# Performance work log

Measured on AMD Instinct MI355X. Metric: run time of the kernel, lower is better.

The kernel has to match this reference:

```python
import jax, jax.numpy as jnp
import numpy as np

K = 3
TOP_K = 10
MASK_RATIO = 0.5
EPS_COS = 1e-8
EPS_DEG = 1e-6


def setup_inputs() -> dict:
    key = jax.random.key(0)
    ks = jax.random.split(key, 10)
    N, C, H, O, E = 4096, 128, 128, 64, 65536
    x = jax.random.normal(ks[0], (N, C), dtype=jnp.float32)
    edge_index = jax.random.randint(ks[1], (2, E), 0, N, dtype=jnp.int64)
    alpha = jnp.full((K,), 1.0 / K, dtype=jnp.float32)
    fusion_W = 0.02 * jax.random.normal(ks[2], (2 * H, H), dtype=jnp.float32)
    fusion_b = jnp.zeros((H,), dtype=jnp.float32)
    lin0_W = 0.02 * jax.random.normal(ks[3], (C, H), dtype=jnp.float32)
    lin0_b = jnp.zeros((H,), dtype=jnp.float32)
    lin1_W = 0.02 * jax.random.normal(ks[4], (H, O), dtype=jnp.float32)
    lin1_b = jnp.zeros((O,), dtype=jnp.float32)
    return {
        "x": x, "edge_index": edge_index, "alpha": alpha,
        "fusion_W": fusion_W, "fusion_b": fusion_b,
        "lin0_W": lin0_W, "lin0_b": lin0_b,
        "lin1_W": lin1_W, "lin1_b": lin1_b,
    }


def reference(x, edge_index, alpha, fusion_W, fusion_b, lin0_W, lin0_b, lin1_W, lin1_b):
    N = x.shape[0]
    # dense adjacency and its powers: A^0 = I (so A^0 @ x = x), A^1, A^2
    A = jnp.zeros((N, N), x.dtype).at[edge_index[0], edge_index[1]].set(1.0)
    A2 = A @ A
    hop_feats = jnp.stack([x, A @ x, A2 @ x], axis=0)  # [K, N, C]

    # per-node cosine-similarity top-k (self always included, cos=1)
    xn = x / (jnp.linalg.norm(x, axis=-1, keepdims=True) + EPS_COS)
    sim = xn @ xn.T  # [N, N]
    _, topk_idx = jax.lax.top_k(sim, TOP_K)  # [N, TOP_K]

    # random keep-mask per node, forced True at top-k neighbors
    mask = jax.random.uniform(jax.random.key(42), (N, N)) < MASK_RATIO
    rows = jnp.arange(N)[:, None]
    mask = mask.at[rows, topk_idx].set(True)
    Mf = mask.astype(x.dtype)  # [N, N]

    # alpha-weighted multi-hop aggregate, masked mean over selected nodes
    agg = jnp.einsum('k,knc->nc', alpha, hop_feats)  # [N, C]
    fused = (Mf @ agg) / (Mf.sum(axis=1, keepdims=True) + EPS_DEG)  # [N, C]

    h = jnp.concatenate([x, fused], axis=-1) @ fusion_W + fusion_b
    h = jax.nn.relu(h @ lin0_W + lin0_b)  # dropout inactive in eval
    out = h @ lin1_W + lin1_b
    return jax.nn.log_softmax(out, axis=1)
```

## Files before the change

### kernel.cpp

```cpp
#include <hip/hip_runtime.h>
#include <hip/hip_bf16.h>
#include <stdint.h>


#define N_NODES 4096
#define C_DIM   128
#define WPR     128
#define HALF_P  8388608u
#define TOPK    10
#define LSTR    13
#define JSPLIT  4
#define KSPLIT  2

typedef __attribute__((ext_vector_type(8))) short bf16x8;
typedef __attribute__((ext_vector_type(4))) float f32x4;

__device__ __forceinline__ uint16_t f2bf(float f) {
    uint32_t u = __float_as_uint(f);
    return (uint16_t)((u + 0x7FFFu + ((u >> 16) & 1u)) >> 16);
}

__device__ __forceinline__ uint32_t rotl32(uint32_t v, int r) {
    return (v << r) | (v >> (32 - r));
}

__device__ __forceinline__ void threefry2x32(uint32_t k0, uint32_t k1,
                                             uint32_t x0, uint32_t x1,
                                             uint32_t& o0, uint32_t& o1) {
    uint32_t ks2 = k0 ^ k1 ^ 0x1BD11BDAu;
    x0 += k0; x1 += k1;
#define TF_ROUND(r) { x0 += x1; x1 = rotl32(x1, (r)); x1 ^= x0; }
    TF_ROUND(13) TF_ROUND(15) TF_ROUND(26) TF_ROUND(6)
    x0 += k1;  x1 += ks2 + 1u;
    TF_ROUND(17) TF_ROUND(29) TF_ROUND(16) TF_ROUND(24)
    x0 += ks2; x1 += k0 + 2u;
    TF_ROUND(13) TF_ROUND(15) TF_ROUND(26) TF_ROUND(6)
    x0 += k0;  x1 += k1 + 3u;
    TF_ROUND(17) TF_ROUND(29) TF_ROUND(16) TF_ROUND(24)
    x0 += k1;  x1 += ks2 + 4u;
    TF_ROUND(13) TF_ROUND(15) TF_ROUND(26) TF_ROUND(6)
    x0 += ks2; x1 += k0 + 5u;
#undef TF_ROUND
    o0 = x0; o1 = x1;
}

__global__ void scatter_kernel(const int* __restrict__ ei, int E,
                               uint32_t* __restrict__ Abits) {
    __shared__ int cnt_oddnz;
    int t = threadIdx.x;
    if (t == 0) cnt_oddnz = 0;
    __syncthreads();
    if (((const uint32_t*)ei)[2 * t + 1] != 0u) atomicAdd(&cnt_oddnz, 1);
    __syncthreads();
    bool is64 = (cnt_oddnz <= 8);
    int e = blockIdx.x * blockDim.x + t;
    if (e >= E) return;
    int src, dst;
    if (is64) { src = ei[2 * e]; dst = ei[2 * (E + e)]; }
    else      { src = ei[e];     dst = ei[E + e]; }
    src &= (N_NODES - 1);
    dst &= (N_NODES - 1);
    atomicOr(&Abits[src * WPR + (dst >> 5)], 1u << (dst & 31));
}

__global__ void spmm_norm_kernel(const uint32_t* __restrict__ Abits,
                                 const float* __restrict__ xf,
                                 float* __restrict__ hop1,
                                 uint16_t* __restrict__ xnb) {
    int i = blockIdx.x;
    int c = threadIdx.x;
    __shared__ uint32_t wbits[WPR];
    __shared__ float ws[2];
    wbits[c] = Abits[i * WPR + c];
    __syncthreads();
    float acc = 0.f;
    for (int w = 0; w < WPR; ++w) {
        uint32_t bits = wbits[w];
        while (bits) {
            int b = __ffs(bits) - 1;
            bits &= bits - 1;
            acc += xf[(w * 32 + b) * C_DIM + c];
        }
    }
    hop1[i * C_DIM + c] = acc;
    float v = xf[i * C_DIM + c];
    float sq = v * v;
    #pragma unroll
    for (int off = 32; off >= 1; off >>= 1) sq += __shfl_xor(sq, off);
    if ((c & 63) == 0) ws[c >> 6] = sq;
    __syncthreads();
    float tot = ws[0] + ws[1];
    xnb[i * C_DIM + c] = f2bf(v / (sqrtf(tot) + 1e-8f));
}

__launch_bounds__(512, 4)
__global__ void combo_topk_kernel(const uint32_t* __restrict__ Abits,
                                  const float* __restrict__ hop1,
                                  const float* __restrict__ xf,
                                  const float* __restrict__ alpha,
                                  uint16_t* __restrict__ aggTb,
                                  const uint16_t* __restrict__ xnb,
                                  uint32_t* __restrict__ Mbits,
                                  int* __restrict__ degInt,
                                  float* __restrict__ topv,
                                  int* __restrict__ topi) {
    __shared__ uint8_t smem[32 * 16 * LSTR * 6];
    int t = threadIdx.x;

    if (blockIdx.x < 1024) {
        float*    sval = (float*)smem;
        uint16_t* sidx = (uint16_t*)(smem + 32 * 16 * LSTR * 4);
        int it   = blockIdx.x & 255;
        int part = blockIdx.x >> 8;
        int i0 = it * 16;
        int w = t >> 6;
        int lane = t & 63;
        int col = lane & 15;
        int quad = lane >> 4;

        bf16x8 bfi[4];
        #pragma unroll
        for (int s = 0; s < 4; ++s)
            bfi[s] = *(const bf16x8*)&xnb[(size_t)(i0 + col) * C_DIM + s * 32 + quad * 8];

        float tv[TOPK]; int ti[TOPK];
        #pragma unroll
        for (int k = 0; k < TOPK; ++k) { tv[k] = -1e30f; ti[k] = 0xFFFF; }

        int jt0 = part * 64 + w * 8;
        for (int p = 0; p < 8; ++p) {
            int j0 = (jt0 + p) * 16;
            f32x4 acc = {0.f, 0.f, 0.f, 0.f};
            #pragma unroll
            for (int s = 0; s < 4; ++s) {
                bf16x8 aj = *(const bf16x8*)&xnb[(size_t)(j0 + col) * C_DIM + s * 32 + quad * 8];
                acc = __builtin_amdgcn_mfma_f32_16x16x32_bf16(aj, bfi[s], acc, 0, 0, 0);
            }
            float m4 = fmaxf(fmaxf(acc[0], acc[1]), fmaxf(acc[2], acc[3]));
            if (m4 > tv[TOPK-1]) {
                #pragma unroll
                for (int r = 0; r < 4; ++r) {
                    float d = acc[r];
                    if (d > tv[TOPK-1]) {
                        int j = j0 + quad * 4 + r;
                        tv[TOPK-1] = d; ti[TOPK-1] = j;
                        #pragma unroll
                        for (int q = TOPK - 2; q >= 0; --q) {
                            if (tv[q+1] > tv[q]) {
                                float fv = tv[q]; tv[q] = tv[q+1]; tv[q+1] = fv;
                                int iv = ti[q];  ti[q] = ti[q+1];  ti[q+1] = iv;
                            }
                        }
                    }
                }
            }
        }

        int base = ((w * 4 + quad) * 16 + col) * LSTR;
        #pragma unroll
        for (int k = 0; k < TOPK; ++k) {
            sval[base + k] = tv[k];
            sidx[base + k] = (uint16_t)ti[k];
        }

        int row = t & 15, L = t >> 4;
        for (int s = 16; s >= 1; s >>= 1) {
            __syncthreads();
            if (L < s) {
                int la = (L * 16 + row) * LSTR;
                int lb = ((L + s) * 16 + row) * LSTR;
                float ov[TOPK]; uint16_t oi[TOPK];
                int ia = 0, ib = 0;
                #pragma unroll
                for (int k = 0; k < TOPK; ++k) {
                    float va = sval[la + ia], vb = sval[lb + ib];
                    uint16_t xa = sidx[la + ia], xb = sidx[lb + ib];
                    bool takeA = (va > vb) || (va == vb && xa < xb);
                    if (takeA) { ov[k] = va; oi[k] = xa; ++ia; }
                    else       { ov[k] = vb; oi[k] = xb; ++ib; }
                }
                #pragma unroll
                for (int k = 0; k < TOPK; ++k) { sval[la + k] = ov[k]; sidx[la + k] = oi[k]; }
            }
        }
        __syncthreads();
        if (t < 16) {
            size_t gi = (size_t)(part * N_NODES + i0 + t) * TOPK;
            #pragma unroll
            for (int k = 0; k < TOPK; ++k) {
                topv[gi + k] = sval[t * LSTR + k];
                topi[gi + k] = (int)sidx[t * LSTR + k];
            }
        }
    } else {
        uint32_t* wb = (uint32_t*)smem;
        int bid = blockIdx.x - 1024;
        int sg = t >> 7;
        int c  = t & 127;
        int i  = bid * 4 + sg;
        wb[sg * 128 + c] = Abits[i * WPR + c];
        __syncthreads();
        float acc = 0.f;
        for (int w = 0; w < WPR; ++w) {
            uint32_t bits = wb[sg * 128 + w];
            while (bits) {
                int b = __ffs(bits) - 1;
                bits &= bits - 1;
                acc += hop1[(w * 32 + b) * C_DIM + c];
            }
        }
        float xv  = xf[i * C_DIM + c];
        float h1v = hop1[i * C_DIM + c];
        float a = alpha[0] * xv + alpha[1] * h1v + alpha[2] * acc;
        aggTb[(size_t)c * N_NODES + i] = f2bf(a);

        uint32_t u = (uint32_t)(i * 128 + c);
        uint32_t tid = u >> 1;
        uint32_t halfb = u & 1u;
        uint32_t base = tid * 32u + halfb * 16u;
        uint32_t w0 = 0u, w1 = 0u;
        for (int k = 0; k < 16; ++k) {
            uint32_t o0, o1;
            threefry2x32(0u, 42u, base + k, HALF_P + base + k, o0, o1);
            w0 |= (uint32_t)((o0 >> 31) ^ 1u) << k;
            w1 |= (uint32_t)((o1 >> 31) ^ 1u) << k;
        }
        uint32_t w0o = (uint32_t)__shfl_xor((int)w0, 1);
        uint32_t w1o = (uint32_t)__shfl_xor((int)w1, 1);
        int p0 = 0, p1 = 0;
        if (halfb == 0u) {
            uint32_t W0 = w0 | (w0o << 16);
            uint32_t W1 = w1 | (w1o << 16);
            Mbits[tid] = W0;
            Mbits[(HALF_P >> 5) + tid] = W1;
            p0 = __popc(W0); p1 = __popc(W1);
        }
        #pragma unroll
        for (int off = 32; off >= 1; off >>= 1) {
            p0 += __shfl_xor(p0, off);
            p1 += __shfl_xor(p1, off);
        }
        if ((t & 63) == 0) {
            int row0 = i >> 1;
            atomicAdd(&degInt[row0], p0);
            atomicAdd(&degInt[2048 + row0], p1);
        }
    }
}

__launch_bounds__(512, 4)
__global__ void fused_kernel(const uint32_t* __restrict__ Mbits,
                             const uint16_t* __restrict__ aggTb,
                             const float* __restrict__ topv,
                             const int* __restrict__ topi,
                             int* __restrict__ degInt,
                             float* __restrict__ fpart) {
    int i0 = blockIdx.x * 16;
    int part = blockIdx.y;
    int t = threadIdx.x;
    int w = t >> 6;
    int lane = t & 63;
    int col = lane & 15;
    int quad = lane >> 4;

    __shared__ uint32_t smask[16][65];
    __shared__ float    lv[16][JSPLIT][TOPK];
    __shared__ uint16_t li[16][JSPLIT][TOPK];
    for (int r = t; r < 16 * 64; r += 512)
        smask[r >> 6][r & 63] =
            Mbits[(size_t)(i0 + (r >> 6)) * WPR + part * 64 + (r & 63)];
    if (t < 16 * JSPLIT) {
        int row = t & 15, q = t >> 4;
        size_t gi = (size_t)(q * N_NODES + i0 + row) * TOPK;
        #pragma unroll
        for (int k = 0; k < TOPK; ++k) {
            lv[row][q][k] = topv[gi + k];
            li[row][q][k] = (uint16_t)topi[gi + k];
        }
    }
    __syncthreads();

    if (t < 16) {
        int ix[JSPLIT] = {0, 0, 0, 0};
        int newc = 0;
        int kw0 = part * 2048;
        #pragma unroll
        for (int k = 0; k < TOPK; ++k) {
            float bestv = -1e38f; int bestj = 0x7fffffff; int bestq = 0;
            #pragma unroll
            for (int q = 0; q < JSPLIT; ++q) {
                bool ok = ix[q] < TOPK;
                float fv = ok ? lv[t][q][ix[q]] : -1e38f;
                int   jj = ok ? (int)li[t][q][ix[q]] : 0x7fffffff;
                if (fv > bestv || (fv == bestv && jj < bestj)) {
                    bestv = fv; bestj = jj; bestq = q;
                }
            }
            ++ix[bestq];
            int rel = bestj - kw0;
            if (rel >= 0 && rel < 2048) {
                uint32_t* wp = &smask[t][rel >> 5];
                uint32_t old = *wp, bit = 1u << (bestj & 31);
                newc += (int)((old & bit) == 0u);
                *wp = old | bit;
            }
        }
        if (newc) atomicAdd(&degInt[i0 + t], newc);
    }
    __syncthreads();

    const uint16_t* brow = aggTb + (size_t)(w * 16 + col) * N_NODES;
    int kbase = part * 2048;
    f32x4 acc[4];
    #pragma unroll
    for (int u = 0; u < 4; ++u) acc[u] = (f32x4){0.f, 0.f, 0.f, 0.f};

    for (int k0 = 0; k0 < 2048; k0 += 128) {
        #pragma unroll
        for (int u = 0; u < 4; ++u) {
            uint32_t mw = smask[col][(k0 >> 5) + u];
            uint32_t byte = (mw >> (quad * 8)) & 0xFFu;
            union { uint32_t uu[4]; bf16x8 v; } a;
            #pragma unroll
            for (int pp = 0; pp < 4; ++pp) {
                uint32_t lo = (byte >> (2 * pp)) & 1u;
                uint32_t hi = (byte >> (2 * pp + 1)) & 1u;
                a.uu[pp] = (lo ? 0x3F80u : 0u) | (hi ? 0x3F800000u : 0u);
            }
            bf16x8 b = *(const bf16x8*)&brow[kbase + k0 + u * 32 + quad * 8];
            acc[u] = __builtin_amdgcn_mfma_f32_16x16x32_bf16(a.v, b, acc[u], 0, 0, 0);
        }
    }
    #pragma unroll
    for (int r = 0; r < 4; ++r) {
        int il = quad * 4 + r;
        float s = (acc[0][r] + acc[1][r]) + (acc[2][r] + acc[3][r]);
        fpart[(size_t)part * (N_NODES * C_DIM)
              + (size_t)(i0 + il) * C_DIM + w * 16 + col] = s;
    }
}

__global__ void mlp_kernel(const float* __restrict__ xf,
                           const float* __restrict__ fpart,
                           const int* __restrict__ degInt,
                           const float* __restrict__ fW, const float* __restrict__ fB,
                           const float* __restrict__ l0W, const float* __restrict__ l0B,
                           const float* __restrict__ l1W, const float* __restrict__ l1B,
                           float* __restrict__ out) {
    int i0 = blockIdx.x * 4;
    int t = threadIdx.x;
    __shared__ float lx[4][256];
    __shared__ float hb[4][128];
    const float* f0 = fpart;
    const float* f1 = fpart + (size_t)N_NODES * C_DIM;
    for (int r = t; r < 4 * 128; r += 128) {
        int row = r >> 7, c = r & 127;
        size_t idx = (size_t)(i0 + row) * C_DIM + c;
        lx[row][c] = xf[idx];
        lx[row][128 + c] = (f0[idx] + f1[idx])
                           / ((float)degInt[i0 + row] + 1e-6f);
    }
    __syncthreads();
    float acc[4];
    #pragma unroll
    for (int r = 0; r < 4; ++r) acc[r] = fB[t];
    for (int k = 0; k < 256; ++k) {
        float wv = fW[k * 128 + t];
        #pragma unroll
        for (int r = 0; r < 4; ++r) acc[r] = fmaf(lx[r][k], wv, acc[r]);
    }
    #pragma unroll
    for (int r = 0; r < 4; ++r) hb[r][t] = acc[r];
    __syncthreads();
    #pragma unroll
    for (int r = 0; r < 4; ++r) acc[r] = l0B[t];
    for (int k = 0; k < 128; ++k) {
        float wv = l0W[k * 128 + t];
        #pragma unroll
        for (int r = 0; r < 4; ++r) acc[r] = fmaf(hb[r][k], wv, acc[r]);
    }
    __syncthreads();
    #pragma unroll
    for (int r = 0; r < 4; ++r) lx[r][t] = fmaxf(acc[r], 0.f);
    __syncthreads();
    int o = t & 63, pr = t >> 6;
    #pragma unroll
    for (int rr = 0; rr < 2; ++rr) {
        int r = pr + 2 * rr;
        float a = l1B[o];
        for (int k = 0; k < 128; ++k)
            a = fmaf(lx[r][k], l1W[k * 64 + o], a);
        float m = a;
        #pragma unroll
        for (int off = 32; off >= 1; off >>= 1) m = fmaxf(m, __shfl_xor(m, off));
        float e = expf(a - m);
        float s = e;
        #pragma unroll
        for (int off = 32; off >= 1; off >>= 1) s += __shfl_xor(s, off);
        out[(size_t)(i0 + r) * 64 + o] = a - m - logf(s);
    }
}

extern "C" void kernel_launch(void* const* d_in, const int* in_sizes, int n_in,
                              void* d_out, int out_size, void* d_ws, size_t ws_size,
                              hipStream_t stream) {
    const float* xf    = (const float*)d_in[0];
    const int*   ei    = (const int*)d_in[1];
    const float* alpha = (const float*)d_in[2];
    const float* fW    = (const float*)d_in[3];
    const float* fB    = (const float*)d_in[4];
    const float* l0W   = (const float*)d_in[5];
    const float* l0B   = (const float*)d_in[6];
    const float* l1W   = (const float*)d_in[7];
    const float* l1B   = (const float*)d_in[8];
    float* out = (float*)d_out;
    const int E  = in_sizes[1] / 2;
    const int NC = N_NODES * C_DIM;

    char* p = (char*)d_ws;
    const size_t SZ = (size_t)NC * 4;
    uint32_t* Abits  = (uint32_t*)p; p += SZ;
    int*      degInt = (int*)p;      p += N_NODES * 4;
    float*    hop1   = (float*)p;    p += SZ;
    uint32_t* Mbits  = (uint32_t*)p; p += SZ;
    float*    fpart  = (float*)p;    p += KSPLIT * SZ;
    uint16_t* xnb    = (uint16_t*)p; p += SZ / 2;
    uint16_t* aggTb  = (uint16_t*)p; p += SZ / 2;
    float*    topv   = (float*)p;    p += (size_t)JSPLIT * N_NODES * TOPK * 4;
    int*      topi   = (int*)p;      p += (size_t)JSPLIT * N_NODES * TOPK * 4;

    hipMemsetAsync(Abits, 0, SZ + N_NODES * 4, stream);
    scatter_kernel<<<(E + 255) / 256, 256, 0, stream>>>(ei, E, Abits);
    spmm_norm_kernel<<<N_NODES, 128, 0, stream>>>(Abits, xf, hop1, xnb);
    combo_topk_kernel<<<2048, 512, 0, stream>>>(Abits, hop1, xf, alpha,
                                                aggTb, xnb, Mbits, degInt,
                                                topv, topi);
    fused_kernel<<<dim3(N_NODES / 16, KSPLIT), 512, 0, stream>>>(Mbits, aggTb,
                                                                 topv, topi,
                                                                 degInt, fpart);
    mlp_kernel<<<N_NODES / 4, 128, 0, stream>>>(xf, fpart, degInt,
                                                fW, fB, l0W, l0B, l1W, l1B, out);
}
```

Baseline: 226.6 us.

## Merge memset, scatter, spmm and combo/topk into one cooperative kernel

Replaces the memset, scatter, first-hop SpMM/normalize and combo/topk launches with a single cooperative mega-kernel of 1024 blocks that uses grid.sync between phases. The aim is to remove launch and inter-kernel gaps. In exchange, the topk and hop2 phases, previously split across 2048 blocks, now run sequentially within each block. The launch bounds rise to 8 waves so all blocks can be co-resident, which risks register pressure in the topk code, and grid-wide barriers add their own cost.

```diff
diff --git a/kernel.cpp b/kernel.cpp
--- a/kernel.cpp
+++ b/kernel.cpp
@@ -1,7 +1,10 @@
 #include <hip/hip_runtime.h>
 #include <hip/hip_bf16.h>
+#include <hip/hip_cooperative_groups.h>
 #include <stdint.h>
 
+
+namespace cg = cooperative_groups;
 
 #define N_NODES 4096
 #define C_DIM   128
@@ -44,74 +47,83 @@
     o0 = x0; o1 = x1;
 }
 
-__global__ void scatter_kernel(const int* __restrict__ ei, int E,
-                               uint32_t* __restrict__ Abits) {
+__launch_bounds__(512, 8)
+__global__ void mega_kernel(const int* __restrict__ ei, int E,
+                            const float* __restrict__ xf,
+                            const float* __restrict__ alpha,
+                            uint32_t* __restrict__ Abits,
+                            int* __restrict__ degInt,
+                            float* __restrict__ hop1,
+                            uint16_t* __restrict__ xnb,
+                            uint16_t* __restrict__ aggTb,
+                            uint32_t* __restrict__ Mbits,
+                            float* __restrict__ topv,
+                            int* __restrict__ topi) {
+    cg::grid_group grid = cg::this_grid();
+    __shared__ uint8_t smem[32 * 16 * LSTR * 6];
+    __shared__ float ws4[4][2];
     __shared__ int cnt_oddnz;
     int t = threadIdx.x;
-    if (t == 0) cnt_oddnz = 0;
-    __syncthreads();
-    if (((const uint32_t*)ei)[2 * t + 1] != 0u) atomicAdd(&cnt_oddnz, 1);
-    __syncthreads();
-    bool is64 = (cnt_oddnz <= 8);
-    int e = blockIdx.x * blockDim.x + t;
-    if (e >= E) return;
-    int src, dst;
-    if (is64) { src = ei[2 * e]; dst = ei[2 * (E + e)]; }
-    else      { src = ei[e];     dst = ei[E + e]; }
-    src &= (N_NODES - 1);
-    dst &= (N_NODES - 1);
-    atomicOr(&Abits[src * WPR + (dst >> 5)], 1u << (dst & 31));
-}
-
-__global__ void spmm_norm_kernel(const uint32_t* __restrict__ Abits,
-                                 const float* __restrict__ xf,
-                                 float* __restrict__ hop1,
-                                 uint16_t* __restrict__ xnb) {
-    int i = blockIdx.x;
-    int c = threadIdx.x;
-    __shared__ uint32_t wbits[WPR];
-    __shared__ float ws[2];
-    wbits[c] = Abits[i * WPR + c];
-    __syncthreads();
-    float acc = 0.f;
-    for (int w = 0; w < WPR; ++w) {
-        uint32_t bits = wbits[w];
-        while (bits) {
-            int b = __ffs(bits) - 1;
-            bits &= bits - 1;
-            acc += xf[(w * 32 + b) * C_DIM + c];
-        }
-    }
-    hop1[i * C_DIM + c] = acc;
-    float v = xf[i * C_DIM + c];
-    float sq = v * v;
-    #pragma unroll
-    for (int off = 32; off >= 1; off >>= 1) sq += __shfl_xor(sq, off);
-    if ((c & 63) == 0) ws[c >> 6] = sq;
-    __syncthreads();
-    float tot = ws[0] + ws[1];
-    xnb[i * C_DIM + c] = f2bf(v / (sqrtf(tot) + 1e-8f));
-}
-
-__launch_bounds__(512, 4)
-__global__ void combo_topk_kernel(const uint32_t* __restrict__ Abits,
-                                  const float* __restrict__ hop1,
-                                  const float* __restrict__ xf,
-                                  const float* __restrict__ alpha,
-                                  uint16_t* __restrict__ aggTb,
-                                  const uint16_t* __restrict__ xnb,
-                                  uint32_t* __restrict__ Mbits,
-                                  int* __restrict__ degInt,
-                                  float* __restrict__ topv,
-                                  int* __restrict__ topi) {
-    __shared__ uint8_t smem[32 * 16 * LSTR * 6];
-    int t = threadIdx.x;
-
-    if (blockIdx.x < 1024) {
+    int b = blockIdx.x;
+
+    {
+        int total = N_NODES * WPR + N_NODES;
+        for (int idx = b * 512 + t; idx < total; idx += 1024 * 512)
+            Abits[idx] = 0u;
+    }
+    grid.sync();
+
+    {
+        if (t == 0) cnt_oddnz = 0;
+        __syncthreads();
+        if (t < 256 && ((const uint32_t*)ei)[2 * t + 1] != 0u)
+            atomicAdd(&cnt_oddnz, 1);
+        __syncthreads();
+        bool is64 = (cnt_oddnz <= 8);
+        int e = b * 64 + t;
+        if (t < 64 && e < E) {
+            int src, dst;
+            if (is64) { src = ei[2 * e]; dst = ei[2 * (E + e)]; }
+            else      { src = ei[e];     dst = ei[E + e]; }
+            src &= (N_NODES - 1);
+            dst &= (N_NODES - 1);
+            atomicOr(&Abits[src * WPR + (dst >> 5)], 1u << (dst & 31));
+        }
+    }
+    grid.sync();
+
+    {
+        uint32_t* wb = (uint32_t*)smem;
+        int sg = t >> 7, c = t & 127;
+        int i = b * 4 + sg;
+        wb[sg * 128 + c] = Abits[i * WPR + c];
+        __syncthreads();
+        float acc = 0.f;
+        for (int w = 0; w < WPR; ++w) {
+            uint32_t bits = wb[sg * 128 + w];
+            while (bits) {
+                int bb = __ffs(bits) - 1;
+                bits &= bits - 1;
+                acc += xf[(w * 32 + bb) * C_DIM + c];
+            }
+        }
+        hop1[i * C_DIM + c] = acc;
+        float v = xf[i * C_DIM + c];
+        float sq = v * v;
+        #pragma unroll
+        for (int off = 32; off >= 1; off >>= 1) sq += __shfl_xor(sq, off);
+        if ((c & 63) == 0) ws4[sg][c >> 6] = sq;
+        __syncthreads();
+        float tot = ws4[sg][0] + ws4[sg][1];
+        xnb[i * C_DIM + c] = f2bf(v / (sqrtf(tot) + 1e-8f));
+    }
+    grid.sync();
+
+    {
         float*    sval = (float*)smem;
         uint16_t* sidx = (uint16_t*)(smem + 32 * 16 * LSTR * 4);
-        int it   = blockIdx.x & 255;
-        int part = blockIdx.x >> 8;
+        int it   = b & 255;
+        int part = b >> 8;
         int i0 = it * 16;
         int w = t >> 6;
         int lane = t & 63;
@@ -192,21 +204,23 @@
                 topi[gi + k] = (int)sidx[t * LSTR + k];
             }
         }
-    } else {
+        __syncthreads();
+    }
+
+    {
         uint32_t* wb = (uint32_t*)smem;
-        int bid = blockIdx.x - 1024;
         int sg = t >> 7;
         int c  = t & 127;
-        int i  = bid * 4 + sg;
+        int i  = b * 4 + sg;
         wb[sg * 128 + c] = Abits[i * WPR + c];
         __syncthreads();
         float acc = 0.f;
         for (int w = 0; w < WPR; ++w) {
             uint32_t bits = wb[sg * 128 + w];
             while (bits) {
-                int b = __ffs(bits) - 1;
+                int bb = __ffs(bits) - 1;
                 bits &= bits - 1;
-                acc += hop1[(w * 32 + b) * C_DIM + c];
+                acc += hop1[(w * 32 + bb) * C_DIM + c];
             }
         }
         float xv  = xf[i * C_DIM + c];
@@ -327,8 +341,8 @@
                 uint32_t hi = (byte >> (2 * pp + 1)) & 1u;
                 a.uu[pp] = (lo ? 0x3F80u : 0u) | (hi ? 0x3F800000u : 0u);
             }
-            bf16x8 b = *(const bf16x8*)&brow[kbase + k0 + u * 32 + quad * 8];
-            acc[u] = __builtin_amdgcn_mfma_f32_16x16x32_bf16(a.v, b, acc[u], 0, 0, 0);
+            bf16x8 bvec = *(const bf16x8*)&brow[kbase + k0 + u * 32 + quad * 8];
+            acc[u] = __builtin_amdgcn_mfma_f32_16x16x32_bf16(a.v, bvec, acc[u], 0, 0, 0);
         }
     }
     #pragma unroll
@@ -404,8 +418,8 @@
 extern "C" void kernel_launch(void* const* d_in, const int* in_sizes, int n_in,
                               void* d_out, int out_size, void* d_ws, size_t ws_size,
                               hipStream_t stream) {
+    const int*   ei    = (const int*)d_in[1];
     const float* xf    = (const float*)d_in[0];
-    const int*   ei    = (const int*)d_in[1];
     const float* alpha = (const float*)d_in[2];
     const float* fW    = (const float*)d_in[3];
     const float* fB    = (const float*)d_in[4];
@@ -414,7 +428,7 @@
     const float* l1W   = (const float*)d_in[7];
     const float* l1B   = (const float*)d_in[8];
     float* out = (float*)d_out;
-    const int E  = in_sizes[1] / 2;
+    int E  = in_sizes[1] / 2;
     const int NC = N_NODES * C_DIM;
 
     char* p = (char*)d_ws;
@@ -429,12 +443,13 @@
     float*    topv   = (float*)p;    p += (size_t)JSPLIT * N_NODES * TOPK * 4;
     int*      topi   = (int*)p;      p += (size_t)JSPLIT * N_NODES * TOPK * 4;
 
-    hipMemsetAsync(Abits, 0, SZ + N_NODES * 4, stream);
-    scatter_kernel<<<(E + 255) / 256, 256, 0, stream>>>(ei, E, Abits);
-    spmm_norm_kernel<<<N_NODES, 128, 0, stream>>>(Abits, xf, hop1, xnb);
-    combo_topk_kernel<<<2048, 512, 0, stream>>>(Abits, hop1, xf, alpha,
-                                                aggTb, xnb, Mbits, degInt,
-                                                topv, topi);
+    void* args[] = {
+        (void*)&ei, (void*)&E, (void*)&xf, (void*)&alpha,
+        (void*)&Abits, (void*)&degInt, (void*)&hop1, (void*)&xnb,
+        (void*)&aggTb, (void*)&Mbits, (void*)&topv, (void*)&topi
+    };
+    hipLaunchCooperativeKernel((const void*)mega_kernel,
+                               dim3(1024), dim3(512), args, 0, stream);
     fused_kernel<<<dim3(N_NODES / 16, KSPLIT), 512, 0, stream>>>(Mbits, aggTb,
                                                                  topv, topi,
                                                                  degInt, fpart);
```

Measured after the change: 543.0 us. 140% more time.
